# Optimization experiments

Measured on AMD Instinct MI355X. Metric: run time of the kernel, lower is better.

## Reference

```python
import jax, jax.numpy as jnp
import numpy as np


def setup_inputs() -> dict:
    key = jax.random.key(0)
    kc, kh, kx, kwx, kwh = jax.random.split(key, 5)
    B, T, D, H = 64, 512, 1024, 1024
    c0 = jax.random.normal(kc, (B, H), dtype=jnp.float32)
    h0 = jax.random.normal(kh, (B, H), dtype=jnp.float32)
    xs = jax.random.normal(kx, (B, T, D), dtype=jnp.float32)
    # fan-in scaled init like lecun_normal (flax default)
    Wx = jax.random.normal(kwx, (D, 4 * H), dtype=jnp.float32) / np.sqrt(D)
    Wh = jax.random.normal(kwh, (H, 4 * H), dtype=jnp.float32) / np.sqrt(H)
    b = jnp.zeros((4 * H,), dtype=jnp.float32)
    return {"c0": c0, "h0": h0, "xs": xs, "Wx": Wx, "Wh": Wh, "b": b}


def _lstm(c0, h0, xs, Wx, Wh, b):
    # Batch the input-to-hidden projection across all timesteps (compute-dense GEMM)
    xproj = jnp.einsum('btd,dh->tbh', xs, Wx)  # [T, B, 4H], time-major for scan

    def step(carry, xp):
        c, h = carry
        gates = xp + h @ Wh + b                # [B, 4H]
        i, f, g, o = jnp.split(gates, 4, axis=-1)  # flax gate order: i, f, g, o
        new_c = jax.nn.sigmoid(f) * c + jax.nn.sigmoid(i) * jnp.tanh(g)
        new_h = jax.nn.sigmoid(o) * jnp.tanh(new_c)
        return (new_c, new_h), new_h

    (cT, hT), ys = jax.lax.scan(step, (c0, h0), xproj)
    return (cT, hT), jnp.transpose(ys, (1, 0, 2))  # ys back to [B, T, H]


def reference(c0, h0, xs, Wx, Wh, b):
    return _lstm(c0, h0, xs, Wx, Wh, b)
```

## Files before the change

kernel.cpp:

```cpp
#include <hip/hip_runtime.h>


typedef _Float16 half8 __attribute__((ext_vector_type(8)));
typedef float floatx4 __attribute__((ext_vector_type(4)));

__device__ __forceinline__ void gll16(const void* g, void* l) {
  __builtin_amdgcn_global_load_lds(
      (const __attribute__((address_space(1))) unsigned int*)g,
      (__attribute__((address_space(3))) unsigned int*)l, 16, 0, 0);
}

__device__ __forceinline__ float sigm(float x) { return 1.f / (1.f + __expf(-x)); }
__device__ __forceinline__ float tanhfast(float x) { return 1.f - 2.f / (__expf(2.f * x) + 1.f); }

__global__ void prep_ew(const float* __restrict__ xs, const float* __restrict__ h0,
                        _Float16* __restrict__ xs16, _Float16* __restrict__ hb0,
                        int* __restrict__ flags) {
  long gid = (long)blockIdx.x * blockDim.x + threadIdx.x;
  if (gid < 4194304) {
    const float4* p = (const float4*)xs + gid * 2;
    float4 u = p[0], w = p[1];
    half8 o;
    o[0] = (_Float16)u.x; o[1] = (_Float16)u.y; o[2] = (_Float16)u.z; o[3] = (_Float16)u.w;
    o[4] = (_Float16)w.x; o[5] = (_Float16)w.y; o[6] = (_Float16)w.z; o[7] = (_Float16)w.w;
    *(half8*)(xs16 + gid * 8) = o;
  } else if (gid < 4202496) {
    long j = gid - 4194304;
    const float4* p = (const float4*)h0 + j * 2;
    float4 u = p[0], w = p[1];
    half8 o;
    o[0] = (_Float16)u.x; o[1] = (_Float16)u.y; o[2] = (_Float16)u.z; o[3] = (_Float16)u.w;
    o[4] = (_Float16)w.x; o[5] = (_Float16)w.y; o[6] = (_Float16)w.z; o[7] = (_Float16)w.w;
    *(half8*)(hb0 + j * 8) = o;
  } else if (gid < 4202752) {
    flags[gid - 4202496] = 0;
  }
}

__global__ void transpose_k(const float* __restrict__ in, _Float16* __restrict__ outp) {
  __shared__ float s[32][33];
  int bx = blockIdx.x * 32, by = blockIdx.y * 32;
  int tx = threadIdx.x, ty = threadIdx.y;
#pragma unroll
  for (int k = 0; k < 32; k += 8)
    s[ty + k][tx] = in[(long)(by + ty + k) * 4096 + bx + tx];
  __syncthreads();
#pragma unroll
  for (int k = 0; k < 32; k += 8)
    outp[(long)(bx + ty + k) * 1024 + by + tx] = (_Float16)s[tx][ty + k];
}

__global__ __launch_bounds__(256) void gemm1(const _Float16* __restrict__ A,
                                             const _Float16* __restrict__ Bt,
                                             _Float16* __restrict__ C) {
  __shared__ _Float16 sA[4096], sB[4096];
  const int tid = threadIdx.x;
  const int w = tid >> 6, l = tid & 63, li = l & 15, q = l >> 4;
  const int wr = w >> 1, wc = w & 1;
  const int m0 = blockIdx.y * 128, n0 = blockIdx.x * 128;
  floatx4 acc[4][4] = {};
  const _Float16* gA0 = A + (long)(m0 + (w * 16 + li)) * 1024 + q * 8;
  const _Float16* gA1 = A + (long)(m0 + ((4 + w) * 16 + li)) * 1024 + q * 8;
  const _Float16* gB0 = Bt + (long)(n0 + (w * 16 + li)) * 1024 + q * 8;
  const _Float16* gB1 = Bt + (long)(n0 + ((4 + w) * 16 + li)) * 1024 + q * 8;
  _Float16* lA0 = sA + (w * 64) * 8;
  _Float16* lA1 = sA + (256 + w * 64) * 8;
  _Float16* lB0 = sB + (w * 64) * 8;
  _Float16* lB1 = sB + (256 + w * 64) * 8;
  for (int k0 = 0; k0 < 1024; k0 += 32) {
    __syncthreads();
    gll16(gA0 + k0, lA0);
    gll16(gA1 + k0, lA1);
    gll16(gB0 + k0, lB0);
    gll16(gB1 + k0, lB1);
    __syncthreads();
    half8 af[4], bf[4];
    const half8* pA = (const half8*)sA;
    const half8* pB = (const half8*)sB;
#pragma unroll
    for (int i = 0; i < 4; i++) af[i] = pA[(wr * 4 + i) * 64 + l];
#pragma unroll
    for (int j = 0; j < 4; j++) bf[j] = pB[(wc * 4 + j) * 64 + l];
#pragma unroll
    for (int i = 0; i < 4; i++)
#pragma unroll
      for (int j = 0; j < 4; j++)
        acc[i][j] = __builtin_amdgcn_mfma_f32_16x16x32_f16(af[i], bf[j], acc[i][j], 0, 0, 0);
  }
#pragma unroll
  for (int i = 0; i < 4; i++) {
#pragma unroll
    for (int r = 0; r < 4; r++) {
      int m = m0 + wr * 64 + i * 16 + q * 4 + r;
      long orow = (long)(m & 511) * 64 + (m >> 9);
#pragma unroll
      for (int j = 0; j < 4; j++) {
        int gn = n0 + wc * 64 + j * 16 + li;
        C[orow * 4096 + gn] = (_Float16)acc[i][j][r];
      }
    }
  }
}

__global__ __launch_bounds__(256, 1) void rec(const _Float16* __restrict__ xproj,
                                              const _Float16* __restrict__ Wht,
                                              const float* __restrict__ bias,
                                              const float* __restrict__ c0,
                                              _Float16* __restrict__ hbuf,
                                              int* __restrict__ flags,
                                              float* __restrict__ out) {
  __shared__ _Float16 sW[65536];
  const int tid = threadIdx.x;
  const int wgid = blockIdx.x;
  const int v = tid >> 6;
  const int l = tid & 63, li = l & 15, q = l >> 4;
  const int ks = wgid * 16;

#pragma unroll 4
  for (int i = 0; i < 32; i++) {
    int c = i * 256 + tid;
    int g = c >> 11, kk = (c >> 6) & 31;
    int cli = c & 15, cq = (c >> 4) & 3;
    gll16(Wht + (long)((g << 10) + ks + cli) * 1024 + kk * 32 + cq * 8,
          sW + (long)(c - l) * 8);
  }
  float creg[4];
#pragma unroll
  for (int r = 0; r < 4; r++)
    creg[r] = c0[(long)(v * 16 + q * 4 + r) * 1024 + ks + li];
  float bs[4];
#pragma unroll
  for (int g = 0; g < 4; g++) bs[g] = bias[(g << 10) + ks + li];
  __syncthreads();

  const half8* pW = (const half8*)sW;
  const int fbase = 4 * l;

  for (int t = 0; t < 512; t++) {
    const _Float16* xpt = xproj + (long)t * 262144 + ks + li;
    _Float16 xv[4][4];
#pragma unroll
    for (int g = 0; g < 4; g++)
#pragma unroll
      for (int r = 0; r < 4; r++)
        xv[g][r] = xpt[(long)(v * 16 + q * 4 + r) * 4096 + (g << 10)];

    for (;;) {
      int f0 = __hip_atomic_load(&flags[fbase + 0], __ATOMIC_RELAXED, __HIP_MEMORY_SCOPE_AGENT);
      int f1 = __hip_atomic_load(&flags[fbase + 1], __ATOMIC_RELAXED, __HIP_MEMORY_SCOPE_AGENT);
      int f2 = __hip_atomic_load(&flags[fbase + 2], __ATOMIC_RELAXED, __HIP_MEMORY_SCOPE_AGENT);
      int f3 = __hip_atomic_load(&flags[fbase + 3], __ATOMIC_RELAXED, __HIP_MEMORY_SCOPE_AGENT);
      int fm = min(min(f0, f1), min(f2, f3));
      if (__all(fm >= t)) break;
      __builtin_amdgcn_s_sleep(1);
    }
    __builtin_amdgcn_fence(__ATOMIC_ACQUIRE, "workgroup");

    const _Float16* hrow = hbuf + (long)t * 65536 + (long)(v * 16 + li) * 1024 + q * 8;
    floatx4 acc[4] = {};
    half8 ap[8];
#pragma unroll
    for (int p = 0; p < 8; p++) ap[p] = *(const half8*)(hrow + p * 32);
#pragma unroll
    for (int kk = 0; kk < 32; kk++) {
      half8 a = ap[kk & 7];
#pragma unroll
      for (int g = 0; g < 4; g++)
        acc[g] = __builtin_amdgcn_mfma_f32_16x16x32_f16(a, pW[((g * 32 + kk) << 6) + l], acc[g], 0, 0, 0);
      if (kk < 24) ap[kk & 7] = *(const half8*)(hrow + (kk + 8) * 32);
    }

    _Float16* hnext = hbuf + (long)(t + 1) * 65536;
    float hval[4], cval[4];
#pragma unroll
    for (int r = 0; r < 4; r++) {
      float gi = acc[0][r] + (float)xv[0][r] + bs[0];
      float gf = acc[1][r] + (float)xv[1][r] + bs[1];
      float gg = acc[2][r] + (float)xv[2][r] + bs[2];
      float go = acc[3][r] + (float)xv[3][r] + bs[3];
      float cN = sigm(gf) * creg[r] + sigm(gi) * tanhfast(gg);
      creg[r] = cN;
      cval[r] = cN;
      float hN = sigm(go) * tanhfast(cN);
      hval[r] = hN;
      int b = v * 16 + q * 4 + r;
      unsigned short hu = __builtin_bit_cast(unsigned short, (_Float16)hN);
      __hip_atomic_store((unsigned short*)hnext + (long)b * 1024 + ks + li, hu,
                         __ATOMIC_RELAXED, __HIP_MEMORY_SCOPE_AGENT);
    }
    __builtin_amdgcn_s_waitcnt(0);
    if (l == 0)
      __hip_atomic_store(&flags[4 * wgid + v], t + 1, __ATOMIC_RELAXED, __HIP_MEMORY_SCOPE_AGENT);

#pragma unroll
    for (int r = 0; r < 4; r++) {
      int b = v * 16 + q * 4 + r;
      out[131072 + (long)b * 524288 + (long)t * 1024 + ks + li] = hval[r];
      if (t == 511) {
        out[(long)b * 1024 + ks + li] = cval[r];
        out[65536 + (long)b * 1024 + ks + li] = hval[r];
      }
    }
  }
}

extern "C" void kernel_launch(void* const* d_in, const int* in_sizes, int n_in,
                              void* d_out, int out_size, void* d_ws, size_t ws_size,
                              hipStream_t stream) {
  const float* c0 = (const float*)d_in[0];
  const float* h0 = (const float*)d_in[1];
  const float* xs = (const float*)d_in[2];
  const float* Wx = (const float*)d_in[3];
  const float* Wh = (const float*)d_in[4];
  const float* bias = (const float*)d_in[5];
  float* out = (float*)d_out;

  char* ws = (char*)d_ws;
  size_t off = 0;
  _Float16* xs16 = (_Float16*)(ws + off); off += 67108864;
  _Float16* wxt  = (_Float16*)(ws + off); off += 8388608;
  _Float16* wht  = (_Float16*)(ws + off); off += 8388608;
  _Float16* xprj = (_Float16*)(ws + off); off += 268435456;
  _Float16* hbuf = (_Float16*)(ws + off); off += 67239936;
  int* flags     = (int*)(ws + off);      off += 1024;
  if (ws_size < off) return;

  prep_ew<<<16417, 256, 0, stream>>>(xs, h0, xs16, hbuf, flags);
  transpose_k<<<dim3(128, 32), dim3(32, 8), 0, stream>>>(Wx, wxt);
  transpose_k<<<dim3(128, 32), dim3(32, 8), 0, stream>>>(Wh, wht);
  gemm1<<<dim3(32, 256), 256, 0, stream>>>(xs16, wxt, xprj);
  rec<<<64, 256, 0, stream>>>(xprj, wht, bias, c0, hbuf, flags, out);
}
```

Measured before the change: 6.245 ms.

## Fuse input-projection GEMM with recurrence kernel to overlap via per-timestep counters

```diff
diff --git a/kernel.cpp b/kernel.cpp
--- a/kernel.cpp
+++ b/kernel.cpp
@@ -23,7 +23,10 @@
     half8 o;
     o[0] = (_Float16)u.x; o[1] = (_Float16)u.y; o[2] = (_Float16)u.z; o[3] = (_Float16)u.w;
     o[4] = (_Float16)w.x; o[5] = (_Float16)w.y; o[6] = (_Float16)w.z; o[7] = (_Float16)w.w;
-    *(half8*)(xs16 + gid * 8) = o;
+    long e = gid * 8;
+    long row = e >> 10;
+    long b = row >> 9, t = row & 511;
+    *(half8*)(xs16 + ((t << 6) + b) * 1024 + (e & 1023)) = o;
   } else if (gid < 4202496) {
     long j = gid - 4194304;
     const float4* p = (const float4*)h0 + j * 2;
@@ -32,7 +35,7 @@
     o[0] = (_Float16)u.x; o[1] = (_Float16)u.y; o[2] = (_Float16)u.z; o[3] = (_Float16)u.w;
     o[4] = (_Float16)w.x; o[5] = (_Float16)w.y; o[6] = (_Float16)w.z; o[7] = (_Float16)w.w;
     *(half8*)(hb0 + j * 8) = o;
-  } else if (gid < 4202752) {
+  } else if (gid < 4203264) {
     flags[gid - 4202496] = 0;
   }
 }
@@ -50,67 +53,79 @@
     outp[(long)(bx + ty + k) * 1024 + by + tx] = (_Float16)s[tx][ty + k];
 }
 
-__global__ __launch_bounds__(256) void gemm1(const _Float16* __restrict__ A,
-                                             const _Float16* __restrict__ Bt,
-                                             _Float16* __restrict__ C) {
-  __shared__ _Float16 sA[4096], sB[4096];
+__global__ __launch_bounds__(256, 1) void fused(const _Float16* __restrict__ xs16,
+                                                const _Float16* __restrict__ wxt,
+                                                _Float16* __restrict__ xprj,
+                                                const _Float16* __restrict__ wht,
+                                                const float* __restrict__ bias,
+                                                const float* __restrict__ c0,
+                                                _Float16* __restrict__ hbuf,
+                                                int* __restrict__ flags,
+                                                float* __restrict__ out) {
+  __shared__ char smem[131072];
   const int tid = threadIdx.x;
-  const int w = tid >> 6, l = tid & 63, li = l & 15, q = l >> 4;
-  const int wr = w >> 1, wc = w & 1;
-  const int m0 = blockIdx.y * 128, n0 = blockIdx.x * 128;
-  floatx4 acc[4][4] = {};
-  const _Float16* gA0 = A + (long)(m0 + (w * 16 + li)) * 1024 + q * 8;
-  const _Float16* gA1 = A + (long)(m0 + ((4 + w) * 16 + li)) * 1024 + q * 8;
-  const _Float16* gB0 = Bt + (long)(n0 + (w * 16 + li)) * 1024 + q * 8;
-  const _Float16* gB1 = Bt + (long)(n0 + ((4 + w) * 16 + li)) * 1024 + q * 8;
-  _Float16* lA0 = sA + (w * 64) * 8;
-  _Float16* lA1 = sA + (256 + w * 64) * 8;
-  _Float16* lB0 = sB + (w * 64) * 8;
-  _Float16* lB1 = sB + (256 + w * 64) * 8;
-  for (int k0 = 0; k0 < 1024; k0 += 32) {
+  int* const cnt = flags + 256;
+  int* const tot = flags + 512;
+
+  if (blockIdx.x >= 64) {
+    _Float16* sA = (_Float16*)smem;
+    _Float16* sB = (_Float16*)(smem + 8192);
+    const int gid = blockIdx.x - 64;
+    const int by = gid >> 5, bx = gid & 31;
+    const int w = tid >> 6, l = tid & 63, li = l & 15, q = l >> 4;
+    const int wr = w >> 1, wc = w & 1;
+    const int m0 = by * 128, n0 = bx * 128;
+    floatx4 acc[4][4] = {};
+    const _Float16* gA0 = xs16 + (long)(m0 + (w * 16 + li)) * 1024 + q * 8;
+    const _Float16* gA1 = xs16 + (long)(m0 + ((4 + w) * 16 + li)) * 1024 + q * 8;
+    const _Float16* gB0 = wxt + (long)(n0 + (w * 16 + li)) * 1024 + q * 8;
+    const _Float16* gB1 = wxt + (long)(n0 + ((4 + w) * 16 + li)) * 1024 + q * 8;
+    _Float16* lA0 = sA + (w * 64) * 8;
+    _Float16* lA1 = sA + (256 + w * 64) * 8;
+    _Float16* lB0 = sB + (w * 64) * 8;
+    _Float16* lB1 = sB + (256 + w * 64) * 8;
+    for (int k0 = 0; k0 < 1024; k0 += 32) {
+      __syncthreads();
+      gll16(gA0 + k0, lA0);
+      gll16(gA1 + k0, lA1);
+      gll16(gB0 + k0, lB0);
+      gll16(gB1 + k0, lB1);
+      __syncthreads();
+      half8 af[4], bf[4];
+      const half8* pA = (const half8*)sA;
+      const half8* pB = (const half8*)sB;
+#pragma unroll
+      for (int i = 0; i < 4; i++) af[i] = pA[(wr * 4 + i) * 64 + l];
+#pragma unroll
+      for (int j = 0; j < 4; j++) bf[j] = pB[(wc * 4 + j) * 64 + l];
+#pragma unroll
+      for (int i = 0; i < 4; i++)
+#pragma unroll
+        for (int j = 0; j < 4; j++)
+          acc[i][j] = __builtin_amdgcn_mfma_f32_16x16x32_f16(af[i], bf[j], acc[i][j], 0, 0, 0);
+    }
+#pragma unroll
+    for (int i = 0; i < 4; i++) {
+#pragma unroll
+      for (int r = 0; r < 4; r++) {
+        int m = m0 + wr * 64 + i * 16 + q * 4 + r;
+#pragma unroll
+        for (int j = 0; j < 4; j++) {
+          int gn = n0 + wc * 64 + j * 16 + li;
+          xprj[(long)m * 4096 + gn] = (_Float16)acc[i][j][r];
+        }
+      }
+    }
     __syncthreads();
-    gll16(gA0 + k0, lA0);
-    gll16(gA1 + k0, lA1);
-    gll16(gB0 + k0, lB0);
-    gll16(gB1 + k0, lB1);
-    __syncthreads();
-    half8 af[4], bf[4];
-    const half8* pA = (const half8*)sA;
-    const half8* pB = (const half8*)sB;
-#pragma unroll
-    for (int i = 0; i < 4; i++) af[i] = pA[(wr * 4 + i) * 64 + l];
-#pragma unroll
-    for (int j = 0; j < 4; j++) bf[j] = pB[(wc * 4 + j) * 64 + l];
-#pragma unroll
-    for (int i = 0; i < 4; i++)
-#pragma unroll
-      for (int j = 0; j < 4; j++)
-        acc[i][j] = __builtin_amdgcn_mfma_f32_16x16x32_f16(af[i], bf[j], acc[i][j], 0, 0, 0);
-  }
-#pragma unroll
-  for (int i = 0; i < 4; i++) {
-#pragma unroll
-    for (int r = 0; r < 4; r++) {
-      int m = m0 + wr * 64 + i * 16 + q * 4 + r;
-      long orow = (long)(m & 511) * 64 + (m >> 9);
-#pragma unroll
-      for (int j = 0; j < 4; j++) {
-        int gn = n0 + wc * 64 + j * 16 + li;
-        C[orow * 4096 + gn] = (_Float16)acc[i][j][r];
-      }
-    }
-  }
-}
-
-__global__ __launch_bounds__(256, 1) void rec(const _Float16* __restrict__ xproj,
-                                              const _Float16* __restrict__ Wht,
-                                              const float* __restrict__ bias,
-                                              const float* __restrict__ c0,
-                                              _Float16* __restrict__ hbuf,
-                                              int* __restrict__ flags,
-                                              float* __restrict__ out) {
-  __shared__ _Float16 sW[65536];
-  const int tid = threadIdx.x;
+    if (tid == 0) {
+      __builtin_amdgcn_fence(__ATOMIC_RELEASE, "agent");
+      __hip_atomic_fetch_add(&cnt[by], 1, __ATOMIC_RELAXED, __HIP_MEMORY_SCOPE_AGENT);
+      __hip_atomic_fetch_add(tot, 1, __ATOMIC_RELAXED, __HIP_MEMORY_SCOPE_AGENT);
+    }
+    return;
+  }
+
+  _Float16* sW = (_Float16*)smem;
   const int wgid = blockIdx.x;
   const int v = tid >> 6;
   const int l = tid & 63, li = l & 15, q = l >> 4;
@@ -121,7 +136,7 @@
     int c = i * 256 + tid;
     int g = c >> 11, kk = (c >> 6) & 31;
     int cli = c & 15, cq = (c >> 4) & 3;
-    gll16(Wht + (long)((g << 10) + ks + cli) * 1024 + kk * 32 + cq * 8,
+    gll16(wht + (long)((g << 10) + ks + cli) * 1024 + kk * 32 + cq * 8,
           sW + (long)(c - l) * 8);
   }
   float creg[4];
@@ -134,10 +149,22 @@
   __syncthreads();
 
   const half8* pW = (const half8*)sW;
-  const int fbase = 4 * l;
+  const int fidx = 4 * l + v;
+  int xdone = 0;
 
   for (int t = 0; t < 512; t++) {
-    const _Float16* xpt = xproj + (long)t * 262144 + ks + li;
+    if (!xdone && !(t & 1)) {
+      const int nb = t >> 1;
+      for (;;) {
+        int cr = __hip_atomic_load(&cnt[nb], __ATOMIC_RELAXED, __HIP_MEMORY_SCOPE_AGENT);
+        if (cr >= 32) break;
+        __builtin_amdgcn_s_sleep(16);
+      }
+      xdone = (__hip_atomic_load(tot, __ATOMIC_RELAXED, __HIP_MEMORY_SCOPE_AGENT) >= 8192);
+      __builtin_amdgcn_fence(__ATOMIC_ACQUIRE, "agent");
+    }
+
+    const _Float16* xpt = xprj + (long)t * 262144 + ks + li;
     _Float16 xv[4][4];
 #pragma unroll
     for (int g = 0; g < 4; g++)
@@ -146,12 +173,8 @@
         xv[g][r] = xpt[(long)(v * 16 + q * 4 + r) * 4096 + (g << 10)];
 
     for (;;) {
-      int f0 = __hip_atomic_load(&flags[fbase + 0], __ATOMIC_RELAXED, __HIP_MEMORY_SCOPE_AGENT);
-      int f1 = __hip_atomic_load(&flags[fbase + 1], __ATOMIC_RELAXED, __HIP_MEMORY_SCOPE_AGENT);
-      int f2 = __hip_atomic_load(&flags[fbase + 2], __ATOMIC_RELAXED, __HIP_MEMORY_SCOPE_AGENT);
-      int f3 = __hip_atomic_load(&flags[fbase + 3], __ATOMIC_RELAXED, __HIP_MEMORY_SCOPE_AGENT);
-      int fm = min(min(f0, f1), min(f2, f3));
-      if (__all(fm >= t)) break;
+      int f = __hip_atomic_load(&flags[fidx], __ATOMIC_RELAXED, __HIP_MEMORY_SCOPE_AGENT);
+      if (__all(f >= t)) break;
       __builtin_amdgcn_s_sleep(1);
     }
     __builtin_amdgcn_fence(__ATOMIC_ACQUIRE, "workgroup");
@@ -222,12 +245,11 @@
   _Float16* wht  = (_Float16*)(ws + off); off += 8388608;
   _Float16* xprj = (_Float16*)(ws + off); off += 268435456;
   _Float16* hbuf = (_Float16*)(ws + off); off += 67239936;
-  int* flags     = (int*)(ws + off);      off += 1024;
+  int* flags     = (int*)(ws + off);      off += 4096;
   if (ws_size < off) return;
 
-  prep_ew<<<16417, 256, 0, stream>>>(xs, h0, xs16, hbuf, flags);
+  prep_ew<<<16419, 256, 0, stream>>>(xs, h0, xs16, hbuf, flags);
   transpose_k<<<dim3(128, 32), dim3(32, 8), 0, stream>>>(Wx, wxt);
   transpose_k<<<dim3(128, 32), dim3(32, 8), 0, stream>>>(Wh, wht);
-  gemm1<<<dim3(32, 256), 256, 0, stream>>>(xs16, wxt, xprj);
-  rec<<<64, 256, 0, stream>>>(xprj, wht, bias, c0, hbuf, flags, out);
-}
+  fused<<<8256, 256, 0, stream>>>(xs16, wxt, xprj, wht, bias, c0, hbuf, flags, out);
+}
```

Result: faster. 5.930 ms (-5.1%).
